# Optimization experiments

Hardware: AMD Instinct MI355X
Metric: run time of the kernel (lower is better)

## Reference

```python
import jax, jax.numpy as jnp
import numpy as np

H = 2048  # hidden_dim == input_dim


def _lstm_step(x, h, c, Wih, Whh, bih, bhh):
    # x: [1, in], h/c: [1, H]; PyTorch gate order: i, f, g, o along 4H axis
    gates = x @ Wih.T + h @ Whh.T + bih + bhh  # [1, 4H]
    i, f, g, o = jnp.split(gates, 4, axis=-1)
    c2 = jax.nn.sigmoid(f) * c + jax.nn.sigmoid(i) * jnp.tanh(g)
    h2 = jax.nn.sigmoid(o) * jnp.tanh(c2)
    return h2, c2


def setup_inputs() -> dict:
    key = jax.random.key(0)
    ks = jax.random.split(key, 20)
    s = 0.02
    inp = {
        "x": jax.random.normal(ks[0], (1,), dtype=jnp.float32),
        "input_hidden": jax.random.normal(ks[1], (3, 1, H), dtype=jnp.float32),
        "input_cell": jax.random.normal(ks[2], (3, 1, H), dtype=jnp.float32),
        # layer 0: input_size = 1
        "Wih0": jax.random.normal(ks[3], (4 * H, 1), dtype=jnp.float32) * s,
        "Whh0": jax.random.normal(ks[4], (4 * H, H), dtype=jnp.float32) * s,
        "bih0": jax.random.normal(ks[5], (4 * H,), dtype=jnp.float32) * s,
        "bhh0": jax.random.normal(ks[6], (4 * H,), dtype=jnp.float32) * s,
        # layers 1, 2: input_size = H
        "Wih1": jax.random.normal(ks[7], (4 * H, H), dtype=jnp.float32) * s,
        "Whh1": jax.random.normal(ks[8], (4 * H, H), dtype=jnp.float32) * s,
        "bih1": jax.random.normal(ks[9], (4 * H,), dtype=jnp.float32) * s,
        "bhh1": jax.random.normal(ks[10], (4 * H,), dtype=jnp.float32) * s,
        "Wih2": jax.random.normal(ks[11], (4 * H, H), dtype=jnp.float32) * s,
        "Whh2": jax.random.normal(ks[12], (4 * H, H), dtype=jnp.float32) * s,
        "bih2": jax.random.normal(ks[13], (4 * H,), dtype=jnp.float32) * s,
        "bhh2": jax.random.normal(ks[14], (4 * H,), dtype=jnp.float32) * s,
        # output projection: Linear(H, 1)
        "Wout": jax.random.normal(ks[15], (1, H), dtype=jnp.float32) * s,
        "bout": jax.random.normal(ks[16], (1,), dtype=jnp.float32) * s,
    }
    return inp


def reference(x, input_hidden, input_cell,
              Wih0, Whh0, bih0, bhh0,
              Wih1, Whh1, bih1, bhh1,
              Wih2, Whh2, bih2, bhh2,
              Wout, bout):
    # x.reshape((1,1,1)) in torch -> single timestep, batch 1, feature 1
    inp = x.reshape(1, 1)  # [batch=1, in=1]
    params = [(Wih0, Whh0, bih0, bhh0),
              (Wih1, Whh1, bih1, bhh1),
              (Wih2, Whh2, bih2, bhh2)]
    hs, cs = [], []
    layer_in = inp
    for l, (Wih, Whh, bih, bhh) in enumerate(params):  # fixed 3 layers
        h2, c2 = _lstm_step(layer_in, input_hidden[l], input_cell[l], Wih, Whh, bih, bhh)
        hs.append(h2)
        cs.append(c2)
        layer_in = h2
    hidden_n = jnp.stack(hs, axis=0)  # [3, 1, H]
    cell_n = jnp.stack(cs, axis=0)    # [3, 1, H]
    # top-layer output [1,1,H] -> Linear -> [1,1,1]
    y = (layer_in @ Wout.T + bout).reshape(1, 1, 1)
    return y, hidden_n, cell_n
```

## Files before the change

### kernel.cpp

```cpp
#include <hip/hip_runtime.h>
#include <math.h>

#define H 2048

__device__ __forceinline__ float sigmoidf_(float v) {
    return 1.0f / (1.0f + expf(-v));
}

__device__ __forceinline__ float wave_reduce_sum(float v) {
    v += __shfl_down(v, 32, 64);
    v += __shfl_down(v, 16, 64);
    v += __shfl_down(v, 8, 64);
    v += __shfl_down(v, 4, 64);
    v += __shfl_down(v, 2, 64);
    v += __shfl_down(v, 1, 64);
    return v;
}

__global__ __launch_bounds__(256, 2)
void lstm_layer(const float* __restrict__ Wih, const float* __restrict__ Whh,
                const float* __restrict__ bih, const float* __restrict__ bhh,
                const float* __restrict__ xin,
                const float* __restrict__ hin,
                const float* __restrict__ cin,
                float* __restrict__ hout, float* __restrict__ cout)
{
    const int t = blockIdx.x * 4 + (threadIdx.x >> 6);
    const int lane = threadIdx.x & 63;

    float4 xv[8], hv[8];
    const float4* x4 = (const float4*)xin;
    const float4* h4 = (const float4*)hin;
#pragma unroll
    for (int k = 0; k < 8; ++k) {
        xv[k] = x4[lane + 64 * k];
        hv[k] = h4[lane + 64 * k];
    }

    float gsum[4];
#pragma unroll 1
    for (int g = 0; g < 4; ++g) {
        const float4* wi = (const float4*)(Wih + (size_t)(g * H + t) * H);
        const float4* wh = (const float4*)(Whh + (size_t)(g * H + t) * H);
        float ai = 0.0f, ah = 0.0f;
#pragma unroll
        for (int k = 0; k < 8; ++k) {
            float4 a = wi[lane + 64 * k];
            float4 b = wh[lane + 64 * k];
            ai += a.x * xv[k].x + a.y * xv[k].y + a.z * xv[k].z + a.w * xv[k].w;
            ah += b.x * hv[k].x + b.y * hv[k].y + b.z * hv[k].z + b.w * hv[k].w;
        }
        gsum[g] = wave_reduce_sum(ai + ah);
    }

    if (lane == 0) {
        float gi = gsum[0] + bih[t]         + bhh[t];
        float gf = gsum[1] + bih[H + t]     + bhh[H + t];
        float gg = gsum[2] + bih[2 * H + t] + bhh[2 * H + t];
        float go = gsum[3] + bih[3 * H + t] + bhh[3 * H + t];
        float c2 = sigmoidf_(gf) * cin[t] + sigmoidf_(gi) * tanhf(gg);
        float h2 = sigmoidf_(go) * tanhf(c2);
        cout[t] = c2;
        hout[t] = h2;
    }
}

__global__ __launch_bounds__(256, 2)
void lstm_layer0(const float* __restrict__ Wih0,
                 const float* __restrict__ Whh,
                 const float* __restrict__ bih, const float* __restrict__ bhh,
                 const float* __restrict__ xs,
                 const float* __restrict__ hin, const float* __restrict__ cin,
                 float* __restrict__ hout, float* __restrict__ cout)
{
    const int t = blockIdx.x * 4 + (threadIdx.x >> 6);
    const int lane = threadIdx.x & 63;

    float4 hv[8];
    const float4* h4 = (const float4*)hin;
#pragma unroll
    for (int k = 0; k < 8; ++k) hv[k] = h4[lane + 64 * k];

    float gsum[4];
#pragma unroll 1
    for (int g = 0; g < 4; ++g) {
        const float4* wh = (const float4*)(Whh + (size_t)(g * H + t) * H);
        float a0 = 0.0f, a1 = 0.0f;
#pragma unroll
        for (int k = 0; k < 8; k += 2) {
            float4 a = wh[lane + 64 * k];
            float4 b = wh[lane + 64 * (k + 1)];
            a0 += a.x * hv[k].x + a.y * hv[k].y + a.z * hv[k].z + a.w * hv[k].w;
            a1 += b.x * hv[k+1].x + b.y * hv[k+1].y + b.z * hv[k+1].z + b.w * hv[k+1].w;
        }
        gsum[g] = wave_reduce_sum(a0 + a1);
    }

    if (lane == 0) {
        const float x = xs[0];
        float gi = gsum[0] + x * Wih0[t]         + bih[t]         + bhh[t];
        float gf = gsum[1] + x * Wih0[H + t]     + bih[H + t]     + bhh[H + t];
        float gg = gsum[2] + x * Wih0[2 * H + t] + bih[2 * H + t] + bhh[2 * H + t];
        float go = gsum[3] + x * Wih0[3 * H + t] + bih[3 * H + t] + bhh[3 * H + t];
        float c2 = sigmoidf_(gf) * cin[t] + sigmoidf_(gi) * tanhf(gg);
        float h2 = sigmoidf_(go) * tanhf(c2);
        cout[t] = c2;
        hout[t] = h2;
    }
}

__global__ __launch_bounds__(256)
void out_proj(const float* __restrict__ Wout,
              const float* __restrict__ bout,
              const float* __restrict__ h,
              float* __restrict__ y)
{
    __shared__ float partl[4];
    const int tid = threadIdx.x;
    const float4* W4 = (const float4*)Wout;
    const float4* h4 = (const float4*)h;
    float acc = 0.0f;
#pragma unroll
    for (int k = 0; k < 2; ++k) {
        int i = tid + 256 * k;
        float4 a = W4[i];
        float4 b = h4[i];
        acc += a.x * b.x + a.y * b.y + a.z * b.z + a.w * b.w;
    }
    acc = wave_reduce_sum(acc);
    if ((tid & 63) == 0) partl[tid >> 6] = acc;
    __syncthreads();
    if (tid == 0) y[0] = partl[0] + partl[1] + partl[2] + partl[3] + bout[0];
}

extern "C" void kernel_launch(void* const* d_in, const int* in_sizes, int n_in,
                              void* d_out, int out_size, void* d_ws, size_t ws_size,
                              hipStream_t stream) {
    const float* x    = (const float*)d_in[0];
    const float* hin  = (const float*)d_in[1];
    const float* cin  = (const float*)d_in[2];
    const float* Wih0 = (const float*)d_in[3];
    const float* Whh0 = (const float*)d_in[4];
    const float* bih0 = (const float*)d_in[5];
    const float* bhh0 = (const float*)d_in[6];
    const float* Wih1 = (const float*)d_in[7];
    const float* Whh1 = (const float*)d_in[8];
    const float* bih1 = (const float*)d_in[9];
    const float* bhh1 = (const float*)d_in[10];
    const float* Wih2 = (const float*)d_in[11];
    const float* Whh2 = (const float*)d_in[12];
    const float* bih2 = (const float*)d_in[13];
    const float* bhh2 = (const float*)d_in[14];
    const float* Wout = (const float*)d_in[15];
    const float* bout = (const float*)d_in[16];

    float* out = (float*)d_out;
    float* y  = out;
    float* hN = out + 1;
    float* cN = out + 1 + 3 * H;

    lstm_layer0<<<512, 256, 0, stream>>>(Wih0, Whh0, bih0, bhh0, x,
                                         hin, cin, hN, cN);
    lstm_layer<<<512, 256, 0, stream>>>(Wih1, Whh1, bih1, bhh1,
                                        hN, hin + H, cin + H,
                                        hN + H, cN + H);
    lstm_layer<<<512, 256, 0, stream>>>(Wih2, Whh2, bih2, bhh2,
                                        hN + H, hin + 2 * H, cin + 2 * H,
                                        hN + 2 * H, cN + 2 * H);
    out_proj<<<1, 256, 0, stream>>>(Wout, bout, hN + 2 * H, y);
}
```

Measured before the change: 319.3 us.

## Fuse all LSTM layers into one cooperative kernel with early recurrent matvecs

Replaces the four separate launches with a single cooperative kernel that uses grid-wide syncs between layers. The recurrent Whh matvecs for layers 1 and 2 depend only on the input hidden states, so they are computed up front in the first phase. After each sync, only the Wih matvec on the previous layer's output is left to do. This removes launch gaps and shortens the serial dependency chain, at the cost of grid.sync overhead and a smaller grid (256 blocks of 512 threads) that must stay co-resident.

```diff
diff --git a/kernel.cpp b/kernel.cpp
--- a/kernel.cpp
+++ b/kernel.cpp
@@ -1,5 +1,8 @@
 #include <hip/hip_runtime.h>
+#include <hip/hip_cooperative_groups.h>
 #include <math.h>
+
+namespace cg = cooperative_groups;
 
 #define H 2048
 
@@ -17,120 +20,169 @@
     return v;
 }
 
-__global__ __launch_bounds__(256, 2)
-void lstm_layer(const float* __restrict__ Wih, const float* __restrict__ Whh,
-                const float* __restrict__ bih, const float* __restrict__ bhh,
-                const float* __restrict__ xin,
-                const float* __restrict__ hin,
-                const float* __restrict__ cin,
-                float* __restrict__ hout, float* __restrict__ cout)
+__global__ __launch_bounds__(512, 2)
+void lstm_all(const float* __restrict__ xs,
+              const float* __restrict__ hin,
+              const float* __restrict__ cin,
+              const float* __restrict__ Wih0,
+              const float* __restrict__ Whh0,
+              const float* __restrict__ bih0, const float* __restrict__ bhh0,
+              const float* __restrict__ Wih1, const float* __restrict__ Whh1,
+              const float* __restrict__ bih1, const float* __restrict__ bhh1,
+              const float* __restrict__ Wih2, const float* __restrict__ Whh2,
+              const float* __restrict__ bih2, const float* __restrict__ bhh2,
+              const float* __restrict__ Wout, const float* __restrict__ bout,
+              float* __restrict__ out,
+              float* __restrict__ hws)
 {
-    const int t = blockIdx.x * 4 + (threadIdx.x >> 6);
+    cg::grid_group grid = cg::this_grid();
+    const int wid  = threadIdx.x >> 6;
     const int lane = threadIdx.x & 63;
-
-    float4 xv[8], hv[8];
-    const float4* x4 = (const float4*)xin;
-    const float4* h4 = (const float4*)hin;
-#pragma unroll
-    for (int k = 0; k < 8; ++k) {
-        xv[k] = x4[lane + 64 * k];
-        hv[k] = h4[lane + 64 * k];
-    }
-
-    float gsum[4];
-#pragma unroll 1
-    for (int g = 0; g < 4; ++g) {
-        const float4* wi = (const float4*)(Wih + (size_t)(g * H + t) * H);
-        const float4* wh = (const float4*)(Whh + (size_t)(g * H + t) * H);
-        float ai = 0.0f, ah = 0.0f;
-#pragma unroll
-        for (int k = 0; k < 8; ++k) {
-            float4 a = wi[lane + 64 * k];
-            float4 b = wh[lane + 64 * k];
-            ai += a.x * xv[k].x + a.y * xv[k].y + a.z * xv[k].z + a.w * xv[k].w;
-            ah += b.x * hv[k].x + b.y * hv[k].y + b.z * hv[k].z + b.w * hv[k].w;
-        }
-        gsum[g] = wave_reduce_sum(ai + ah);
-    }
-
-    if (lane == 0) {
-        float gi = gsum[0] + bih[t]         + bhh[t];
-        float gf = gsum[1] + bih[H + t]     + bhh[H + t];
-        float gg = gsum[2] + bih[2 * H + t] + bhh[2 * H + t];
-        float go = gsum[3] + bih[3 * H + t] + bhh[3 * H + t];
-        float c2 = sigmoidf_(gf) * cin[t] + sigmoidf_(gi) * tanhf(gg);
-        float h2 = sigmoidf_(go) * tanhf(c2);
-        cout[t] = c2;
-        hout[t] = h2;
-    }
-}
-
-__global__ __launch_bounds__(256, 2)
-void lstm_layer0(const float* __restrict__ Wih0,
-                 const float* __restrict__ Whh,
-                 const float* __restrict__ bih, const float* __restrict__ bhh,
-                 const float* __restrict__ xs,
-                 const float* __restrict__ hin, const float* __restrict__ cin,
-                 float* __restrict__ hout, float* __restrict__ cout)
-{
-    const int t = blockIdx.x * 4 + (threadIdx.x >> 6);
-    const int lane = threadIdx.x & 63;
-
-    float4 hv[8];
-    const float4* h4 = (const float4*)hin;
-#pragma unroll
-    for (int k = 0; k < 8; ++k) hv[k] = h4[lane + 64 * k];
-
-    float gsum[4];
-#pragma unroll 1
-    for (int g = 0; g < 4; ++g) {
-        const float4* wh = (const float4*)(Whh + (size_t)(g * H + t) * H);
-        float a0 = 0.0f, a1 = 0.0f;
-#pragma unroll
-        for (int k = 0; k < 8; k += 2) {
-            float4 a = wh[lane + 64 * k];
-            float4 b = wh[lane + 64 * (k + 1)];
-            a0 += a.x * hv[k].x + a.y * hv[k].y + a.z * hv[k].z + a.w * hv[k].w;
-            a1 += b.x * hv[k+1].x + b.y * hv[k+1].y + b.z * hv[k+1].z + b.w * hv[k+1].w;
-        }
-        gsum[g] = wave_reduce_sum(a0 + a1);
-    }
-
-    if (lane == 0) {
-        const float x = xs[0];
-        float gi = gsum[0] + x * Wih0[t]         + bih[t]         + bhh[t];
-        float gf = gsum[1] + x * Wih0[H + t]     + bih[H + t]     + bhh[H + t];
-        float gg = gsum[2] + x * Wih0[2 * H + t] + bih[2 * H + t] + bhh[2 * H + t];
-        float go = gsum[3] + x * Wih0[3 * H + t] + bih[3 * H + t] + bhh[3 * H + t];
-        float c2 = sigmoidf_(gf) * cin[t] + sigmoidf_(gi) * tanhf(gg);
-        float h2 = sigmoidf_(go) * tanhf(c2);
-        cout[t] = c2;
-        hout[t] = h2;
-    }
-}
-
-__global__ __launch_bounds__(256)
-void out_proj(const float* __restrict__ Wout,
-              const float* __restrict__ bout,
-              const float* __restrict__ h,
-              float* __restrict__ y)
-{
-    __shared__ float partl[4];
-    const int tid = threadIdx.x;
-    const float4* W4 = (const float4*)Wout;
-    const float4* h4 = (const float4*)h;
-    float acc = 0.0f;
-#pragma unroll
-    for (int k = 0; k < 2; ++k) {
-        int i = tid + 256 * k;
-        float4 a = W4[i];
-        float4 b = h4[i];
-        acc += a.x * b.x + a.y * b.y + a.z * b.z + a.w * b.w;
-    }
-    acc = wave_reduce_sum(acc);
-    if ((tid & 63) == 0) partl[tid >> 6] = acc;
-    __syncthreads();
-    if (tid == 0) y[0] = partl[0] + partl[1] + partl[2] + partl[3] + bout[0];
+    const int t    = blockIdx.x * 8 + wid;
+
+    float* yout = out;
+    float* hN   = out + 1;
+    float* cN   = out + 1 + 3 * H;
+
+    float p1[4], p2[4];
+
+    {
+        float4 hv[8];
+        const float4* h4 = (const float4*)hin;
+#pragma unroll
+        for (int k = 0; k < 8; ++k) hv[k] = h4[lane + 64 * k];
+
+        float g0[4];
+#pragma unroll 1
+        for (int g = 0; g < 4; ++g) {
+            const float4* wr = (const float4*)(Whh0 + (size_t)(g * H + t) * H);
+            float a = 0.0f;
+#pragma unroll
+            for (int k = 0; k < 8; ++k) {
+                float4 w = wr[lane + 64 * k];
+                a += w.x * hv[k].x + w.y * hv[k].y + w.z * hv[k].z + w.w * hv[k].w;
+            }
+            g0[g] = wave_reduce_sum(a);
+        }
+        if (lane == 0) {
+            const float x = xs[0];
+            float gi = g0[0] + x * Wih0[t]         + bih0[t]         + bhh0[t];
+            float gf = g0[1] + x * Wih0[H + t]     + bih0[H + t]     + bhh0[H + t];
+            float gg = g0[2] + x * Wih0[2 * H + t] + bih0[2 * H + t] + bhh0[2 * H + t];
+            float go = g0[3] + x * Wih0[3 * H + t] + bih0[3 * H + t] + bhh0[3 * H + t];
+            float c2 = sigmoidf_(gf) * cin[t] + sigmoidf_(gi) * tanhf(gg);
+            float h2 = sigmoidf_(go) * tanhf(c2);
+            cN[t] = c2; hN[t] = h2; hws[t] = h2;
+        }
+
+        h4 = (const float4*)(hin + H);
+#pragma unroll
+        for (int k = 0; k < 8; ++k) hv[k] = h4[lane + 64 * k];
+#pragma unroll 1
+        for (int g = 0; g < 4; ++g) {
+            const float4* wr = (const float4*)(Whh1 + (size_t)(g * H + t) * H);
+            float a = 0.0f;
+#pragma unroll
+            for (int k = 0; k < 8; ++k) {
+                float4 w = wr[lane + 64 * k];
+                a += w.x * hv[k].x + w.y * hv[k].y + w.z * hv[k].z + w.w * hv[k].w;
+            }
+            p1[g] = wave_reduce_sum(a);
+        }
+
+        h4 = (const float4*)(hin + 2 * H);
+#pragma unroll
+        for (int k = 0; k < 8; ++k) hv[k] = h4[lane + 64 * k];
+#pragma unroll 1
+        for (int g = 0; g < 4; ++g) {
+            const float4* wr = (const float4*)(Whh2 + (size_t)(g * H + t) * H);
+            float a = 0.0f;
+#pragma unroll
+            for (int k = 0; k < 8; ++k) {
+                float4 w = wr[lane + 64 * k];
+                a += w.x * hv[k].x + w.y * hv[k].y + w.z * hv[k].z + w.w * hv[k].w;
+            }
+            p2[g] = wave_reduce_sum(a);
+        }
+    }
+    grid.sync();
+
+    {
+        float4 xv[8];
+        const float4* x4 = (const float4*)hws;
+#pragma unroll
+        for (int k = 0; k < 8; ++k) xv[k] = x4[lane + 64 * k];
+        float s[4];
+#pragma unroll 1
+        for (int g = 0; g < 4; ++g) {
+            const float4* wr = (const float4*)(Wih1 + (size_t)(g * H + t) * H);
+            float a = 0.0f;
+#pragma unroll
+            for (int k = 0; k < 8; ++k) {
+                float4 w = wr[lane + 64 * k];
+                a += w.x * xv[k].x + w.y * xv[k].y + w.z * xv[k].z + w.w * xv[k].w;
+            }
+            s[g] = wave_reduce_sum(a);
+        }
+        if (lane == 0) {
+            float gi = s[0] + p1[0] + bih1[t]         + bhh1[t];
+            float gf = s[1] + p1[1] + bih1[H + t]     + bhh1[H + t];
+            float gg = s[2] + p1[2] + bih1[2 * H + t] + bhh1[2 * H + t];
+            float go = s[3] + p1[3] + bih1[3 * H + t] + bhh1[3 * H + t];
+            float c2 = sigmoidf_(gf) * cin[H + t] + sigmoidf_(gi) * tanhf(gg);
+            float h2 = sigmoidf_(go) * tanhf(c2);
+            cN[H + t] = c2; hN[H + t] = h2; hws[H + t] = h2;
+        }
+    }
+    grid.sync();
+
+    {
+        float4 xv[8];
+        const float4* x4 = (const float4*)(hws + H);
+#pragma unroll
+        for (int k = 0; k < 8; ++k) xv[k] = x4[lane + 64 * k];
+        float s[4];
+#pragma unroll 1
+        for (int g = 0; g < 4; ++g) {
+            const float4* wr = (const float4*)(Wih2 + (size_t)(g * H + t) * H);
+            float a = 0.0f;
+#pragma unroll
+            for (int k = 0; k < 8; ++k) {
+                float4 w = wr[lane + 64 * k];
+                a += w.x * xv[k].x + w.y * xv[k].y + w.z * xv[k].z + w.w * xv[k].w;
+            }
+            s[g] = wave_reduce_sum(a);
+        }
+        if (lane == 0) {
+            float gi = s[0] + p2[0] + bih2[t]         + bhh2[t];
+            float gf = s[1] + p2[1] + bih2[H + t]     + bhh2[H + t];
+            float gg = s[2] + p2[2] + bih2[2 * H + t] + bhh2[2 * H + t];
+            float go = s[3] + p2[3] + bih2[3 * H + t] + bhh2[3 * H + t];
+            float c2 = sigmoidf_(gf) * cin[2 * H + t] + sigmoidf_(gi) * tanhf(gg);
+            float h2 = sigmoidf_(go) * tanhf(c2);
+            cN[2 * H + t] = c2; hN[2 * H + t] = h2; hws[2 * H + t] = h2;
+        }
+    }
+    grid.sync();
+
+    if (blockIdx.x == 0) {
+        __shared__ float partl[8];
+        const int tid = threadIdx.x;
+        const float4* W4 = (const float4*)Wout;
+        const float4* h4 = (const float4*)(hws + 2 * H);
+        float4 a = W4[tid];
+        float4 b = h4[tid];
+        float acc = a.x * b.x + a.y * b.y + a.z * b.z + a.w * b.w;
+        acc = wave_reduce_sum(acc);
+        if (lane == 0) partl[wid] = acc;
+        __syncthreads();
+        if (tid == 0) {
+            float s = bout[0];
+#pragma unroll
+            for (int i = 0; i < 8; ++i) s += partl[i];
+            yout[0] = s;
+        }
+    }
 }
 
 extern "C" void kernel_launch(void* const* d_in, const int* in_sizes, int n_in,
@@ -155,17 +207,16 @@
     const float* bout = (const float*)d_in[16];
 
     float* out = (float*)d_out;
-    float* y  = out;
-    float* hN = out + 1;
-    float* cN = out + 1 + 3 * H;
-
-    lstm_layer0<<<512, 256, 0, stream>>>(Wih0, Whh0, bih0, bhh0, x,
-                                         hin, cin, hN, cN);
-    lstm_layer<<<512, 256, 0, stream>>>(Wih1, Whh1, bih1, bhh1,
-                                        hN, hin + H, cin + H,
-                                        hN + H, cN + H);
-    lstm_layer<<<512, 256, 0, stream>>>(Wih2, Whh2, bih2, bhh2,
-                                        hN + H, hin + 2 * H, cin + 2 * H,
-                                        hN + 2 * H, cN + 2 * H);
-    out_proj<<<1, 256, 0, stream>>>(Wout, bout, hN + 2 * H, y);
-}
+    float* hws = (float*)d_ws;
+
+    void* args[] = {
+        (void*)&x, (void*)&hin, (void*)&cin,
+        (void*)&Wih0, (void*)&Whh0, (void*)&bih0, (void*)&bhh0,
+        (void*)&Wih1, (void*)&Whh1, (void*)&bih1, (void*)&bhh1,
+        (void*)&Wih2, (void*)&Whh2, (void*)&bih2, (void*)&bhh2,
+        (void*)&Wout, (void*)&bout,
+        (void*)&out, (void*)&hws
+    };
+    hipLaunchCooperativeKernel((void*)lstm_all, dim3(256), dim3(512),
+                               args, 0, stream);
+}
```

After: 439.4 us. 37.6% more time.
